# Kernel tuning notes

Measured on AMD Instinct MI355X. Metric: run time of the kernel, lower is better.

## Reference

```python
import jax, jax.numpy as jnp
import numpy as np

INFINITY = 1000000000000000.0


def setup_inputs() -> dict:
    key = jax.random.key(0)
    ks = jax.random.split(key, 6)
    B, Lq, Lk = 8, 256, 256
    Dq, Dk, A = 512, 512, 256
    Q = jax.random.normal(ks[0], (B, Lq, 1, Dq), dtype=jnp.float32)
    K = jax.random.normal(ks[1], (B, 1, Lk, Dk), dtype=jnp.float32)
    mask = jax.random.randint(ks[2], (B, Lq, Lk), 0, 2, dtype=jnp.int32)
    W1 = jax.random.normal(ks[3], (A, Dq), dtype=jnp.float32) / np.sqrt(Dq)
    W2 = jax.random.normal(ks[4], (A, Dk), dtype=jnp.float32) / np.sqrt(Dk)
    w3 = jax.random.normal(ks[5], (A,), dtype=jnp.float32) / np.sqrt(A)
    return {"Q": Q, "K": K, "mask": mask, "W1": W1, "W2": W2, "w3": w3}


def reference(Q, K, mask, W1, W2, w3):
    # Project then broadcast-add: [B,Lq,1,A] + [B,1,Lk,A] -> [B,Lq,Lk,A]
    q_proj = jnp.einsum('blqd,ad->blqa', Q, W1)  # [B,Lq,1,A]
    k_proj = jnp.einsum('bqkd,ad->bqka', K, W2)  # [B,1,Lk,A]
    score = jnp.einsum('blka,a->blk', jnp.tanh(q_proj + k_proj), w3)  # [B,Lq,Lk]
    score = jnp.where(mask == 0, -INFINITY, score)
    return jax.nn.softmax(score, axis=-1)
```

## Files before the change

kernel.cpp:

```cpp
#include <hip/hip_runtime.h>
#include <hip/hip_bf16.h>
#include <cstdint>

constexpr int B  = 8;
constexpr int LQ = 256;
constexpr int LK = 256;
constexpr int D  = 512;
constexpr int A  = 256;

constexpr float NEG_INF   = -1e15f;
constexpr float LOG2E     = 1.4426950408889634f;
constexpr float TWO_LOG2E = 2.8853900817779268f;

constexpr int QP_ELEMS = B * LQ * A;
constexpr int XROWS    = 4096;
constexpr int WROWS    = 512;

constexpr int BM  = 64;
constexpr int BN  = 32;
constexpr int BKC = 64;
constexpr int LDK = 72;

typedef short bf16x8 __attribute__((ext_vector_type(8)));
typedef float f32x4  __attribute__((ext_vector_type(4)));

__device__ inline void split2(float x0, float x1, unsigned& hi, unsigned& lo) {
    unsigned u0 = __float_as_uint(x0), u1 = __float_as_uint(x1);
    unsigned h0 = u0 & 0xFFFF0000u, h1 = u1 & 0xFFFF0000u;
    hi = h1 | (u0 >> 16);
    float l0 = x0 - __uint_as_float(h0);
    float l1 = x1 - __uint_as_float(h1);
    lo = (__float_as_uint(l1) & 0xFFFF0000u) | (__float_as_uint(l0) >> 16);
}

__device__ inline void cvt8(float4 a, float4 b, uint4& hi, uint4& lo) {
    split2(a.x, a.y, hi.x, lo.x);
    split2(a.z, a.w, hi.y, lo.y);
    split2(b.x, b.y, hi.z, lo.z);
    split2(b.z, b.w, hi.w, lo.w);
}

__global__ __launch_bounds__(256) void split_pass(const float* __restrict__ Q,
                                                  const float* __restrict__ Kin,
                                                  const float* __restrict__ W1,
                                                  const float* __restrict__ W2,
                                                  ushort* __restrict__ XH,
                                                  ushort* __restrict__ XL,
                                                  ushort* __restrict__ WH,
                                                  ushort* __restrict__ WL) {
    const int XTH = (XROWS * D) / 8;
    int g = blockIdx.x * 256 + threadIdx.x;
    if (g < XTH) {
        int base = g * 8;
        int row = base >> 9, k = base & 511;
        const float* src = (row < 2048) ? (Q + (size_t)row * D + k)
                                        : (Kin + (size_t)(row - 2048) * D + k);
        float4 a = *(const float4*)src;
        float4 b = *(const float4*)(src + 4);
        uint4 h, l;
        cvt8(a, b, h, l);
        *(uint4*)&XH[base] = h;
        *(uint4*)&XL[base] = l;
    } else {
        int base = (g - XTH) * 8;
        int row = base >> 9, k = base & 511;
        const float* src = (row < 256) ? (W1 + (size_t)row * D + k)
                                       : (W2 + (size_t)(row - 256) * D + k);
        float4 a = *(const float4*)src;
        float4 b = *(const float4*)(src + 4);
        uint4 h, l;
        cvt8(a, b, h, l);
        *(uint4*)&WH[base] = h;
        *(uint4*)&WL[base] = l;
    }
}

__global__ __launch_bounds__(256) void proj_gemm(const ushort* __restrict__ XH,
                                                 const ushort* __restrict__ XL,
                                                 const ushort* __restrict__ WH,
                                                 const ushort* __restrict__ WL,
                                                 float* __restrict__ qp,
                                                 float* __restrict__ kp) {
    __shared__ ushort AH[BM][LDK], AL[BM][LDK];
    __shared__ ushort BH[BN][LDK], BL[BN][LDK];

    const int t    = threadIdx.x;
    const int lane = t & 63;
    const int wave = t >> 6;
    const int wm   = (wave >> 1) * 32;
    const int wn   = (wave & 1) * 16;
    const int l15  = lane & 15;
    const int lg   = lane >> 4;

    const int tile_n  = blockIdx.x & 7;
    const int tile_m  = blockIdx.x >> 3;
    const int rowbase = tile_m * BM;
    const int cbase   = tile_n * BN;
    const bool isQ    = rowbase < 2048;

    const int sxm = t >> 2;
    const int sxk = (t & 3) * 16;
    const int swm = t >> 3;
    const int swk = (t & 7) * 8;

    const ushort* xh = XH + (size_t)(rowbase + sxm) * D;
    const ushort* xl = XL + (size_t)(rowbase + sxm) * D;
    const int wrow = (isQ ? 0 : 256) + cbase + swm;
    const ushort* wh = WH + (size_t)wrow * D;
    const ushort* wl = WL + (size_t)wrow * D;

    f32x4 acc[2] = {{0.f, 0.f, 0.f, 0.f}, {0.f, 0.f, 0.f, 0.f}};

    for (int k0 = 0; k0 < D; k0 += BKC) {
        uint4 vxh0 = *(const uint4*)&xh[k0 + sxk];
        uint4 vxh1 = *(const uint4*)&xh[k0 + sxk + 8];
        uint4 vxl0 = *(const uint4*)&xl[k0 + sxk];
        uint4 vxl1 = *(const uint4*)&xl[k0 + sxk + 8];
        uint4 vwh  = *(const uint4*)&wh[k0 + swk];
        uint4 vwl  = *(const uint4*)&wl[k0 + swk];

        __syncthreads();

        *(uint4*)&AH[sxm][sxk]     = vxh0;
        *(uint4*)&AH[sxm][sxk + 8] = vxh1;
        *(uint4*)&AL[sxm][sxk]     = vxl0;
        *(uint4*)&AL[sxm][sxk + 8] = vxl1;
        *(uint4*)&BH[swm][swk]     = vwh;
        *(uint4*)&BL[swm][swk]     = vwl;

        __syncthreads();

#pragma unroll
        for (int ks = 0; ks < BKC; ks += 32) {
            const int kf = ks + lg * 8;
            bf16x8 ah0 = *(const bf16x8*)&AH[wm + l15][kf];
            bf16x8 ah1 = *(const bf16x8*)&AH[wm + 16 + l15][kf];
            bf16x8 al0 = *(const bf16x8*)&AL[wm + l15][kf];
            bf16x8 al1 = *(const bf16x8*)&AL[wm + 16 + l15][kf];
            bf16x8 bh  = *(const bf16x8*)&BH[wn + l15][kf];
            bf16x8 bl  = *(const bf16x8*)&BL[wn + l15][kf];

            acc[0] = __builtin_amdgcn_mfma_f32_16x16x32_bf16(ah0, bh, acc[0], 0, 0, 0);
            acc[1] = __builtin_amdgcn_mfma_f32_16x16x32_bf16(ah1, bh, acc[1], 0, 0, 0);
            acc[0] = __builtin_amdgcn_mfma_f32_16x16x32_bf16(ah0, bl, acc[0], 0, 0, 0);
            acc[1] = __builtin_amdgcn_mfma_f32_16x16x32_bf16(ah1, bl, acc[1], 0, 0, 0);
            acc[0] = __builtin_amdgcn_mfma_f32_16x16x32_bf16(al0, bh, acc[0], 0, 0, 0);
            acc[1] = __builtin_amdgcn_mfma_f32_16x16x32_bf16(al1, bh, acc[1], 0, 0, 0);
        }
    }

    float ex[2][4];
#pragma unroll
    for (int mi = 0; mi < 2; ++mi)
#pragma unroll
        for (int r = 0; r < 4; ++r)
            ex[mi][r] = __builtin_amdgcn_exp2f(acc[mi][r] * TWO_LOG2E);

    if (isQ) {
#pragma unroll
        for (int mi = 0; mi < 2; ++mi)
#pragma unroll
            for (int r = 0; r < 4; ++r) {
                int row = rowbase + wm + mi * 16 + lg * 4 + r;
                int col = cbase + wn + l15;
                qp[(size_t)row * A + col] = ex[mi][r];
            }
    } else {
        __syncthreads();
        float* T = (float*)&AH[0][0];
#pragma unroll
        for (int mi = 0; mi < 2; ++mi)
#pragma unroll
            for (int r = 0; r < 4; ++r) {
                int m = wm + mi * 16 + lg * 4 + r;
                int n = wn + l15;
                T[m * 33 + n] = ex[mi][r];
            }
        __syncthreads();

        const int bb    = (rowbase - 2048) >> 8;
        const int kbase = rowbase & 255;
        float* dstb = kp + (size_t)bb * A * LK;
#pragma unroll
        for (int j = 0; j < 8; ++j) {
            int g  = j * 256 + t;
            int ii = g & 1;
            int kk = (g >> 1) & 63;
            int p  = g >> 7;
            dstb[((size_t)(tile_n * 16 + p) * LK + kbase + kk) * 2 + ii] =
                T[kk * 33 + 2 * p + ii];
        }
    }
}

__global__ __launch_bounds__(256) void score_softmax(const float* __restrict__ qp,
                                                     const float* __restrict__ kpT,
                                                     const int* __restrict__ mask,
                                                     const float* __restrict__ w3,
                                                     float* __restrict__ out) {
    const int t    = threadIdx.x;
    const int row0 = blockIdx.x * 4;
    const int b    = row0 >> 8;

    const float* kpb = kpT + (size_t)b * A * LK;
    const float* q0  = qp + (size_t)row0 * A;

    float acc0 = 0.f, acc1 = 0.f, acc2 = 0.f, acc3 = 0.f;

#pragma unroll 8
    for (int a = 0; a < A; a += 2) {
        float2 ek = *(const float2*)(kpb + ((size_t)(a >> 1) * LK + t) * 2);
        float w0  = w3[a], w1 = w3[a + 1];
        float q0a = q0[a],         q0b = q0[a + 1];
        float q1a = q0[A + a],     q1b = q0[A + a + 1];
        float q2a = q0[2 * A + a], q2b = q0[2 * A + a + 1];
        float q3a = q0[3 * A + a], q3b = q0[3 * A + a + 1];

        float f0 = 1.0f + q0a * ek.x;
        float f1 = 1.0f + q1a * ek.x;
        float f2 = 1.0f + q2a * ek.x;
        float f3 = 1.0f + q3a * ek.x;
        float rA = __builtin_amdgcn_rcpf(f0 * f1);
        float rB = __builtin_amdgcn_rcpf(f2 * f3);
        acc0 = fmaf(f1 * rA, w0, acc0);
        acc1 = fmaf(f0 * rA, w0, acc1);
        acc2 = fmaf(f3 * rB, w0, acc2);
        acc3 = fmaf(f2 * rB, w0, acc3);

        float g0 = 1.0f + q0b * ek.y;
        float g1 = 1.0f + q1b * ek.y;
        float g2 = 1.0f + q2b * ek.y;
        float g3 = 1.0f + q3b * ek.y;
        float rC = __builtin_amdgcn_rcpf(g0 * g1);
        float rD = __builtin_amdgcn_rcpf(g2 * g3);
        acc0 = fmaf(g1 * rC, w1, acc0);
        acc1 = fmaf(g0 * rC, w1, acc1);
        acc2 = fmaf(g3 * rD, w1, acc2);
        acc3 = fmaf(g2 * rD, w1, acc3);
    }

    const int* mrow = mask + (size_t)row0 * LK;
    float sc0 = (mrow[t]          == 0) ? NEG_INF : -2.0f * acc0;
    float sc1 = (mrow[LK + t]     == 0) ? NEG_INF : -2.0f * acc1;
    float sc2 = (mrow[2 * LK + t] == 0) ? NEG_INF : -2.0f * acc2;
    float sc3 = (mrow[3 * LK + t] == 0) ? NEG_INF : -2.0f * acc3;

    __shared__ float red[4][8];
    const int wave = t >> 6, lane = t & 63;

    float m0 = sc0, m1 = sc1, m2 = sc2, m3 = sc3;
#pragma unroll
    for (int off = 32; off > 0; off >>= 1) {
        m0 = fmaxf(m0, __shfl_xor(m0, off));
        m1 = fmaxf(m1, __shfl_xor(m1, off));
        m2 = fmaxf(m2, __shfl_xor(m2, off));
        m3 = fmaxf(m3, __shfl_xor(m3, off));
    }
    if (lane == 0) {
        red[0][wave] = m0; red[1][wave] = m1;
        red[2][wave] = m2; red[3][wave] = m3;
    }
    __syncthreads();
    float rmax0 = fmaxf(fmaxf(red[0][0], red[0][1]), fmaxf(red[0][2], red[0][3]));
    float rmax1 = fmaxf(fmaxf(red[1][0], red[1][1]), fmaxf(red[1][2], red[1][3]));
    float rmax2 = fmaxf(fmaxf(red[2][0], red[2][1]), fmaxf(red[2][2], red[2][3]));
    float rmax3 = fmaxf(fmaxf(red[3][0], red[3][1]), fmaxf(red[3][2], red[3][3]));
    __syncthreads();

    float p0 = __builtin_amdgcn_exp2f((sc0 - rmax0) * LOG2E);
    float p1 = __builtin_amdgcn_exp2f((sc1 - rmax1) * LOG2E);
    float p2 = __builtin_amdgcn_exp2f((sc2 - rmax2) * LOG2E);
    float p3 = __builtin_amdgcn_exp2f((sc3 - rmax3) * LOG2E);

    float s0 = p0, s1 = p1, s2 = p2, s3 = p3;
#pragma unroll
    for (int off = 32; off > 0; off >>= 1) {
        s0 += __shfl_xor(s0, off);
        s1 += __shfl_xor(s1, off);
        s2 += __shfl_xor(s2, off);
        s3 += __shfl_xor(s3, off);
    }
    if (lane == 0) {
        red[0][wave] = s0; red[1][wave] = s1;
        red[2][wave] = s2; red[3][wave] = s3;
    }
    __syncthreads();
    float sum0 = (red[0][0] + red[0][1]) + (red[0][2] + red[0][3]);
    float sum1 = (red[1][0] + red[1][1]) + (red[1][2] + red[1][3]);
    float sum2 = (red[2][0] + red[2][1]) + (red[2][2] + red[2][3]);
    float sum3 = (red[3][0] + red[3][1]) + (red[3][2] + red[3][3]);

    out[(size_t)row0 * LK + t]       = p0 * __builtin_amdgcn_rcpf(sum0);
    out[(size_t)(row0 + 1) * LK + t] = p1 * __builtin_amdgcn_rcpf(sum1);
    out[(size_t)(row0 + 2) * LK + t] = p2 * __builtin_amdgcn_rcpf(sum2);
    out[(size_t)(row0 + 3) * LK + t] = p3 * __builtin_amdgcn_rcpf(sum3);
}

extern "C" void kernel_launch(void* const* d_in, const int* in_sizes, int n_in,
                              void* d_out, int out_size, void* d_ws, size_t ws_size,
                              hipStream_t stream) {
    const float* Q    = (const float*)d_in[0];
    const float* K    = (const float*)d_in[1];
    const int*   mask = (const int*)d_in[2];
    const float* W1   = (const float*)d_in[3];
    const float* W2   = (const float*)d_in[4];
    const float* w3   = (const float*)d_in[5];
    float* out = (float*)d_out;

    float* ws  = (float*)d_ws;
    float*  qp  = ws;
    float*  kpT = ws + QP_ELEMS;
    ushort* XH  = (ushort*)(ws + 2 * QP_ELEMS);
    ushort* XL  = XH + (size_t)XROWS * D;
    ushort* WH  = XL + (size_t)XROWS * D;
    ushort* WL  = WH + (size_t)WROWS * D;

    const int xblocks = (XROWS * D) / 8 / 256;
    const int wblocks = (WROWS * D) / 8 / 256;
    split_pass<<<xblocks + wblocks, 256, 0, stream>>>(Q, K, W1, W2, XH, XL, WH, WL);
    proj_gemm<<<512, 256, 0, stream>>>(XH, XL, WH, WL, qp, kpT);
    score_softmax<<<(B * LQ) / 4, 256, 0, stream>>>(qp, kpT, mask, w3, out);
}
```

Measured before the change: 46.16 us.

## Load GEMM fragments directly from global memory, drop LDS staging

The projection GEMM stops staging A/B tiles through shared memory. Each lane now loads its bf16x8 MFMA fragments straight from global memory across a fully unrolled K loop, which removes the per-chunk barriers and LDS traffic. In exchange, reuse across waves relies on cache instead of LDS, and the global access pattern is strided per lane. The score kernel's unroll factor is also reduced from 8 to 4.

```diff
diff --git a/kernel.cpp b/kernel.cpp
--- a/kernel.cpp
+++ b/kernel.cpp
@@ -18,8 +18,6 @@
 
 constexpr int BM  = 64;
 constexpr int BN  = 32;
-constexpr int BKC = 64;
-constexpr int LDK = 72;
 
 typedef short bf16x8 __attribute__((ext_vector_type(8)));
 typedef float f32x4  __attribute__((ext_vector_type(4)));
@@ -81,8 +79,7 @@
                                                  const ushort* __restrict__ WL,
                                                  float* __restrict__ qp,
                                                  float* __restrict__ kp) {
-    __shared__ ushort AH[BM][LDK], AL[BM][LDK];
-    __shared__ ushort BH[BN][LDK], BL[BN][LDK];
+    __shared__ float T[64 * 33];
 
     const int t    = threadIdx.x;
     const int lane = t & 63;
@@ -98,55 +95,32 @@
     const int cbase   = tile_n * BN;
     const bool isQ    = rowbase < 2048;
 
-    const int sxm = t >> 2;
-    const int sxk = (t & 3) * 16;
-    const int swm = t >> 3;
-    const int swk = (t & 7) * 8;
-
-    const ushort* xh = XH + (size_t)(rowbase + sxm) * D;
-    const ushort* xl = XL + (size_t)(rowbase + sxm) * D;
-    const int wrow = (isQ ? 0 : 256) + cbase + swm;
-    const ushort* wh = WH + (size_t)wrow * D;
-    const ushort* wl = WL + (size_t)wrow * D;
+    const size_t arow = (size_t)(rowbase + wm + l15) * D + lg * 8;
+    const ushort* xh0 = XH + arow;
+    const ushort* xh1 = XH + arow + (size_t)16 * D;
+    const ushort* xl0 = XL + arow;
+    const ushort* xl1 = XL + arow + (size_t)16 * D;
+    const size_t brow = (size_t)((isQ ? 0 : 256) + cbase + wn + l15) * D + lg * 8;
+    const ushort* wh = WH + brow;
+    const ushort* wl = WL + brow;
 
     f32x4 acc[2] = {{0.f, 0.f, 0.f, 0.f}, {0.f, 0.f, 0.f, 0.f}};
 
-    for (int k0 = 0; k0 < D; k0 += BKC) {
-        uint4 vxh0 = *(const uint4*)&xh[k0 + sxk];
-        uint4 vxh1 = *(const uint4*)&xh[k0 + sxk + 8];
-        uint4 vxl0 = *(const uint4*)&xl[k0 + sxk];
-        uint4 vxl1 = *(const uint4*)&xl[k0 + sxk + 8];
-        uint4 vwh  = *(const uint4*)&wh[k0 + swk];
-        uint4 vwl  = *(const uint4*)&wl[k0 + swk];
-
-        __syncthreads();
-
-        *(uint4*)&AH[sxm][sxk]     = vxh0;
-        *(uint4*)&AH[sxm][sxk + 8] = vxh1;
-        *(uint4*)&AL[sxm][sxk]     = vxl0;
-        *(uint4*)&AL[sxm][sxk + 8] = vxl1;
-        *(uint4*)&BH[swm][swk]     = vwh;
-        *(uint4*)&BL[swm][swk]     = vwl;
-
-        __syncthreads();
-
-#pragma unroll
-        for (int ks = 0; ks < BKC; ks += 32) {
-            const int kf = ks + lg * 8;
-            bf16x8 ah0 = *(const bf16x8*)&AH[wm + l15][kf];
-            bf16x8 ah1 = *(const bf16x8*)&AH[wm + 16 + l15][kf];
-            bf16x8 al0 = *(const bf16x8*)&AL[wm + l15][kf];
-            bf16x8 al1 = *(const bf16x8*)&AL[wm + 16 + l15][kf];
-            bf16x8 bh  = *(const bf16x8*)&BH[wn + l15][kf];
-            bf16x8 bl  = *(const bf16x8*)&BL[wn + l15][kf];
-
-            acc[0] = __builtin_amdgcn_mfma_f32_16x16x32_bf16(ah0, bh, acc[0], 0, 0, 0);
-            acc[1] = __builtin_amdgcn_mfma_f32_16x16x32_bf16(ah1, bh, acc[1], 0, 0, 0);
-            acc[0] = __builtin_amdgcn_mfma_f32_16x16x32_bf16(ah0, bl, acc[0], 0, 0, 0);
-            acc[1] = __builtin_amdgcn_mfma_f32_16x16x32_bf16(ah1, bl, acc[1], 0, 0, 0);
-            acc[0] = __builtin_amdgcn_mfma_f32_16x16x32_bf16(al0, bh, acc[0], 0, 0, 0);
-            acc[1] = __builtin_amdgcn_mfma_f32_16x16x32_bf16(al1, bh, acc[1], 0, 0, 0);
-        }
+#pragma unroll
+    for (int ks = 0; ks < D; ks += 32) {
+        bf16x8 ah0 = *(const bf16x8*)(xh0 + ks);
+        bf16x8 ah1 = *(const bf16x8*)(xh1 + ks);
+        bf16x8 al0 = *(const bf16x8*)(xl0 + ks);
+        bf16x8 al1 = *(const bf16x8*)(xl1 + ks);
+        bf16x8 bh  = *(const bf16x8*)(wh + ks);
+        bf16x8 bl  = *(const bf16x8*)(wl + ks);
+
+        acc[0] = __builtin_amdgcn_mfma_f32_16x16x32_bf16(ah0, bh, acc[0], 0, 0, 0);
+        acc[1] = __builtin_amdgcn_mfma_f32_16x16x32_bf16(ah1, bh, acc[1], 0, 0, 0);
+        acc[0] = __builtin_amdgcn_mfma_f32_16x16x32_bf16(ah0, bl, acc[0], 0, 0, 0);
+        acc[1] = __builtin_amdgcn_mfma_f32_16x16x32_bf16(ah1, bl, acc[1], 0, 0, 0);
+        acc[0] = __builtin_amdgcn_mfma_f32_16x16x32_bf16(al0, bh, acc[0], 0, 0, 0);
+        acc[1] = __builtin_amdgcn_mfma_f32_16x16x32_bf16(al1, bh, acc[1], 0, 0, 0);
     }
 
     float ex[2][4];
@@ -167,7 +141,6 @@
             }
     } else {
         __syncthreads();
-        float* T = (float*)&AH[0][0];
 #pragma unroll
         for (int mi = 0; mi < 2; ++mi)
 #pragma unroll
@@ -207,7 +180,7 @@
 
     float acc0 = 0.f, acc1 = 0.f, acc2 = 0.f, acc3 = 0.f;
 
-#pragma unroll 8
+#pragma unroll 4
     for (int a = 0; a < A; a += 2) {
         float2 ek = *(const float2*)(kpb + ((size_t)(a >> 1) * LK + t) * 2);
         float w0  = w3[a], w1 = w3[a + 1];
```

Measured after the change: 54.85 us. 18.8% more time.
